# Kernel optimization log

Hardware: AMD Instinct MI355X
Metric: run time of the kernel (lower is better)

Reference implementation:

```python
import jax, jax.numpy as jnp
import numpy as np

B, S1, S2, E, P = 8, 2048, 2048, 1024, 1024


def setup_inputs() -> dict:
    key = jax.random.key(0)
    k1, k2, k3, k4, k5 = jax.random.split(key, 5)
    query = jax.random.normal(k1, (B, S1, E), dtype=jnp.float32)
    key_t = jax.random.normal(k2, (B, S2, E), dtype=jnp.float32)
    value = jax.random.normal(k3, (B, S2, E), dtype=jnp.float32)
    # nn.Linear(E, P): weight (P, E), bias (P), shared by q/k/v per the source
    bound = 1.0 / np.sqrt(E)
    W = jax.random.uniform(k4, (P, E), minval=-bound, maxval=bound, dtype=jnp.float32)
    b = jax.random.uniform(k5, (P,), minval=-bound, maxval=bound, dtype=jnp.float32)
    return {"query": query, "key": key_t, "value": value, "W": W, "b": b}


def reference(query, key, value, W, b):
    # Source applies queries_projection to all three inputs.
    q = jnp.einsum("bse,pe->bsp", query, W) + b  # (B,S1,P)
    k = jnp.einsum("bse,pe->bsp", key, W) + b    # (B,S2,P)
    v = jnp.einsum("bse,pe->bsp", value, W) + b  # (B,S2,P)
    scale = 1.0 / jnp.sqrt(jnp.float32(k.shape[-1]))
    scores = jnp.einsum("bqp,bkp->bqk", q, k) * scale  # (B,S1,S2)
    weights = jax.nn.softmax(scores, axis=-1)
    return jnp.einsum("bqk,bkp->bqp", weights, v)  # (B,S1,P)
```

## Files before the change

kernel.cpp:

```cpp
#include <hip/hip_runtime.h>


typedef unsigned short u16;
typedef __bf16 bf16x8 __attribute__((ext_vector_type(8)));
typedef float f32x4 __attribute__((ext_vector_type(4)));

__device__ __forceinline__ float b2f(u16 u) {
    union { unsigned i; float f; } x; x.i = ((unsigned)u) << 16; return x.f;
}
__device__ __forceinline__ u16 f2b(float f) {
    union { float f; unsigned i; } x; x.f = f;
    unsigned r = x.i + 0x7FFFu + ((x.i >> 16) & 1u);
    return (u16)(r >> 16);
}

__global__ __launch_bounds__(256)
void convert_f32_bf16(const float* __restrict__ src, u16* __restrict__ dst, long n)
{
    long i = ((long)blockIdx.x * 256 + threadIdx.x) * 8;
    if (i >= n) return;
    const float4* s = (const float4*)(src + i);
    float4 a = s[0], b = s[1];
    ushort4 lo, hi;
    lo.x = f2b(a.x); lo.y = f2b(a.y); lo.z = f2b(a.z); lo.w = f2b(a.w);
    hi.x = f2b(b.x); hi.y = f2b(b.y); hi.z = f2b(b.z); hi.w = f2b(b.w);
    *(ushort4*)(dst + i) = lo;
    *(ushort4*)(dst + i + 4) = hi;
}

#define BM 128
#define BN 128
#define BK 64

__global__ __launch_bounds__(256)
void gemm_nt(const void* __restrict__ A0, const void* __restrict__ A1,
             const void* __restrict__ A2in, const u16* __restrict__ Bb,
             void* __restrict__ C, const u16* __restrict__ bias,
             int K, float alpha, int mode, int ldc,
             long zA, long zB, long zC, int pw, int ph)
{
    __shared__ __align__(16) u16 lds[2 * BM * BK];
    u16* As = lds;
    u16* Bs = lds + BM * BK;

    const int z = blockIdx.z;
    const u16* Bp = Bb + zB * z;
    const long coff = zC * z;

    const int aF32 = (mode == 5);
    const u16*  Ab  = aF32 ? nullptr : ((const u16*)A0 + zA * z);
    const float* A32 = aF32 ? (const float*)(z == 0 ? A0 : (z == 1 ? A1 : A2in))
                            : nullptr;
    const int em = aF32 ? (z == 2 ? 2 : 0) : mode;

    int tx = blockIdx.x, ty = blockIdx.y;
    if (pw > 0) {
        const int gx = gridDim.x;
        const int lin = ty * gx + tx;
        const int xcd = lin & 7, i = lin >> 3;
        const int pcols = gx / pw;
        const int pr = xcd / pcols, pc = xcd - pr * pcols;
        tx = pc * pw + (i % pw);
        ty = pr * ph + (i / pw);
    }
    const int bm0 = ty * BM;
    const int bn0 = tx * BN;

    const int tid  = threadIdx.x;
    const int wave = tid >> 6, lane = tid & 63;
    const int wm = wave >> 1, wn = wave & 1;
    const int quad = lane >> 4, l15 = lane & 15;
    const int sw = l15 & 7;

    f32x4 acc[4][4];
#pragma unroll
    for (int i = 0; i < 4; i++)
#pragma unroll
        for (int j = 0; j < 4; j++) acc[i][j] = f32x4{0.f, 0.f, 0.f, 0.f};

    const int stg_r  = wave * 8 + (lane >> 3);
    const int stg_cg = ((lane & 7) ^ (lane >> 3)) * 8;
    const int stg_cl = (lane & 7) * 8;

    for (int kt = 0; kt < K; kt += BK) {
#pragma unroll
        for (int i = 0; i < 4; i++) {
            const int r = i * 32 + stg_r;
            __builtin_amdgcn_global_load_lds(
                (const __attribute__((address_space(1))) void*)(Bp + (long)(bn0 + r) * K + kt + stg_cg),
                (__attribute__((address_space(3))) void*)(Bs + r * BK + stg_cl),
                16, 0, 0);
        }
        if (!aF32) {
#pragma unroll
            for (int i = 0; i < 4; i++) {
                const int r = i * 32 + stg_r;
                __builtin_amdgcn_global_load_lds(
                    (const __attribute__((address_space(1))) void*)(Ab + (long)(bm0 + r) * K + kt + stg_cg),
                    (__attribute__((address_space(3))) void*)(As + r * BK + stg_cl),
                    16, 0, 0);
            }
        } else {
#pragma unroll
            for (int i = 0; i < 4; i++) {
                const int r = i * 32 + stg_r;
                const float* s = A32 + (long)(bm0 + r) * K + kt + stg_cg;
                float4 f0 = *(const float4*)s;
                float4 f1 = *(const float4*)(s + 4);
                uint4 pk;
                pk.x = (unsigned)f2b(f0.x) | ((unsigned)f2b(f0.y) << 16);
                pk.y = (unsigned)f2b(f0.z) | ((unsigned)f2b(f0.w) << 16);
                pk.z = (unsigned)f2b(f1.x) | ((unsigned)f2b(f1.y) << 16);
                pk.w = (unsigned)f2b(f1.z) | ((unsigned)f2b(f1.w) << 16);
                *(uint4*)(As + r * BK + stg_cl) = pk;
            }
        }
        __syncthreads();

#pragma unroll
        for (int kk = 0; kk < 2; kk++) {
            bf16x8 af[4], bb[4];
#pragma unroll
            for (int t = 0; t < 4; t++)
                af[t] = *(const bf16x8*)(As + (wm * 64 + t * 16 + l15) * BK
                                             + (((kk * 4 + quad) ^ sw) * 8));
#pragma unroll
            for (int t = 0; t < 4; t++)
                bb[t] = *(const bf16x8*)(Bs + (wn * 64 + t * 16 + l15) * BK
                                             + (((kk * 4 + quad) ^ sw) * 8));
#pragma unroll
            for (int mt = 0; mt < 4; mt++)
#pragma unroll
                for (int nt = 0; nt < 4; nt++)
                    acc[mt][nt] = __builtin_amdgcn_mfma_f32_16x16x32_bf16(
                        af[mt], bb[nt], acc[mt][nt], 0, 0, 0);
        }
        __syncthreads();
    }

#pragma unroll
    for (int mt = 0; mt < 4; mt++) {
        const int row = bm0 + wm * 64 + mt * 16 + quad * 4;
#pragma unroll
        for (int nt = 0; nt < 4; nt++) {
            const int col = bn0 + wn * 64 + nt * 16 + l15;
            const float bv = bias ? b2f(bias[col]) : 0.f;
            f32x4 v = acc[mt][nt];
            float o0 = alpha * v[0] + bv;
            float o1 = alpha * v[1] + bv;
            float o2 = alpha * v[2] + bv;
            float o3 = alpha * v[3] + bv;
            if (em == 2) {
                ushort4 pk;
                pk.x = f2b(o0); pk.y = f2b(o1); pk.z = f2b(o2); pk.w = f2b(o3);
                *(ushort4*)((u16*)C + coff + ((long)(row >> 11) << 21) + ((long)col << 11) + (row & 2047)) = pk;
            } else if (em == 1) {
                float* Cf = (float*)C + coff;
                Cf[(long)(row + 0) * ldc + col] = o0;
                Cf[(long)(row + 1) * ldc + col] = o1;
                Cf[(long)(row + 2) * ldc + col] = o2;
                Cf[(long)(row + 3) * ldc + col] = o3;
            } else {
                u16* Cb = (u16*)C + coff;
                Cb[(long)(row + 0) * ldc + col] = f2b(o0);
                Cb[(long)(row + 1) * ldc + col] = f2b(o1);
                Cb[(long)(row + 2) * ldc + col] = f2b(o2);
                Cb[(long)(row + 3) * ldc + col] = f2b(o3);
            }
        }
    }
}

__global__ __launch_bounds__(256)
void softmax_rows(u16* __restrict__ S)
{
    const long row = blockIdx.x;
    u16* p = S + (row << 11);
    const int tid = threadIdx.x, wave = tid >> 6, lane = tid & 63;

    union { uint4 q; u16 u[8]; } d;
    d.q = ((const uint4*)p)[tid];
    float v[8];
#pragma unroll
    for (int i = 0; i < 8; i++) v[i] = b2f(d.u[i]);

    float m = v[0];
#pragma unroll
    for (int i = 1; i < 8; i++) m = fmaxf(m, v[i]);
#pragma unroll
    for (int o = 32; o; o >>= 1) m = fmaxf(m, __shfl_xor(m, o, 64));
    __shared__ float redm[4], reds[4];
    if (lane == 0) redm[wave] = m;
    __syncthreads();
    m = fmaxf(fmaxf(redm[0], redm[1]), fmaxf(redm[2], redm[3]));

    float e[8], s = 0.f;
#pragma unroll
    for (int i = 0; i < 8; i++) { e[i] = __expf(v[i] - m); s += e[i]; }
#pragma unroll
    for (int o = 32; o; o >>= 1) s += __shfl_xor(s, o, 64);
    if (lane == 0) reds[wave] = s;
    __syncthreads();
    s = reds[0] + reds[1] + reds[2] + reds[3];

    const float inv = 1.f / s;
#pragma unroll
    for (int i = 0; i < 8; i++) d.u[i] = f2b(e[i] * inv);
    ((uint4*)p)[tid] = d.q;
}

extern "C" void kernel_launch(void* const* d_in, const int* in_sizes, int n_in,
                              void* d_out, int out_size, void* d_ws, size_t ws_size,
                              hipStream_t stream) {
    const float* query = (const float*)d_in[0];
    const float* key   = (const float*)d_in[1];
    const float* value = (const float*)d_in[2];
    const float* W     = (const float*)d_in[3];
    const float* bias  = (const float*)d_in[4];
    float* out = (float*)d_out;

    u16* sc  = (u16*)d_ws;
    u16* Wc  = (u16*)d_ws + 16777216L;
    u16* bc  = Wc + 1048576L;
    u16* qb  = (u16*)d_ws + 33554432L;
    u16* kb  = qb + 16777216L;
    u16* vT  = kb + 16777216L;

    const dim3 blk(256);

    convert_f32_bf16<<<dim3(512), blk, 0, stream>>>(W, Wc, 1048576L);
    convert_f32_bf16<<<dim3(1), blk, 0, stream>>>(bias, bc, 1024L);

    gemm_nt<<<dim3(8, 128, 3), blk, 0, stream>>>(query, key, value, Wc, qb, bc,
        1024, 1.f, 5, 1024, 0, 0, 16777216L, 8, 16);

    gemm_nt<<<dim3(16, 16, 8), blk, 0, stream>>>(qb, nullptr, nullptr, kb, sc, nullptr,
        1024, 0.03125f, 0, 2048, 2048L * 1024, 2048L * 1024, 2048L * 2048, 8, 4);

    softmax_rows<<<dim3(16384), blk, 0, stream>>>(sc);

    gemm_nt<<<dim3(8, 16, 8), blk, 0, stream>>>(sc, nullptr, nullptr, vT, out, nullptr,
        2048, 1.f, 1, 1024, 2048L * 2048, 1024L * 2048, 2048L * 1024, 4, 4);
}
```

Measured before the change: 538.9 us.

## Replace GEMM with 256x256 8-wave pipelined kernel and pre-convert inputs to bf16

Replaces the 128x128 single-buffered GEMM with a 256x256-tile, 512-thread kernel. It double-buffers LDS, interleaves global-to-LDS staging with MFMA quarters under explicit barriers and waitcnts, and raises wave priority around the MFMA blocks. The fused fp32-to-bf16 conversion of the projection A operand is dropped. Instead, query, key and value are each converted to bf16 in a separate pass and then projected by their own launch. This aims at higher MFMA utilisation and better data reuse, at the cost of extra conversion traffic, more launches, and far fewer blocks per GEMM.

After: 490.6 us. -9.0%, faster.

```diff
diff --git a/kernel.cpp b/kernel.cpp
--- a/kernel.cpp
+++ b/kernel.cpp
@@ -28,132 +28,165 @@
     *(ushort4*)(dst + i + 4) = hi;
 }
 
-#define BM 128
-#define BN 128
-#define BK 64
-
-__global__ __launch_bounds__(256)
-void gemm_nt(const void* __restrict__ A0, const void* __restrict__ A1,
-             const void* __restrict__ A2in, const u16* __restrict__ Bb,
-             void* __restrict__ C, const u16* __restrict__ bias,
-             int K, float alpha, int mode, int ldc,
-             long zA, long zB, long zC, int pw, int ph)
+
+#define BARX()   __builtin_amdgcn_s_barrier()
+#define WAITL0() asm volatile("s_waitcnt lgkmcnt(0)" ::: "memory")
+#define WV4()    asm volatile("s_waitcnt vmcnt(4)" ::: "memory")
+#define WV0()    asm volatile("s_waitcnt vmcnt(0)" ::: "memory")
+#define PRIO1()  __builtin_amdgcn_s_setprio(1)
+#define PRIO0()  __builtin_amdgcn_s_setprio(0)
+
+__global__ __launch_bounds__(512, 2)
+void gemm8(const u16* __restrict__ A, const u16* __restrict__ B,
+           void* __restrict__ C, const u16* __restrict__ bias,
+           int K, float alpha, int em, int ldc,
+           long zA, long zB, long zC, int pw, int ph)
 {
-    __shared__ __align__(16) u16 lds[2 * BM * BK];
-    u16* As = lds;
-    u16* Bs = lds + BM * BK;
+    __shared__ __align__(16) u16 lds[65536];
 
     const int z = blockIdx.z;
-    const u16* Bp = Bb + zB * z;
+    const u16* Ap = A + zA * z;
+    const u16* Bp = B + zB * z;
     const long coff = zC * z;
-
-    const int aF32 = (mode == 5);
-    const u16*  Ab  = aF32 ? nullptr : ((const u16*)A0 + zA * z);
-    const float* A32 = aF32 ? (const float*)(z == 0 ? A0 : (z == 1 ? A1 : A2in))
-                            : nullptr;
-    const int em = aF32 ? (z == 2 ? 2 : 0) : mode;
 
     int tx = blockIdx.x, ty = blockIdx.y;
     if (pw > 0) {
         const int gx = gridDim.x;
         const int lin = ty * gx + tx;
-        const int xcd = lin & 7, i = lin >> 3;
+        const int xcd = lin & 7, ii = lin >> 3;
         const int pcols = gx / pw;
         const int pr = xcd / pcols, pc = xcd - pr * pcols;
-        tx = pc * pw + (i % pw);
-        ty = pr * ph + (i / pw);
-    }
-    const int bm0 = ty * BM;
-    const int bn0 = tx * BN;
-
-    const int tid  = threadIdx.x;
+        tx = pc * pw + (ii % pw);
+        ty = pr * ph + (ii / pw);
+    }
+    const int bm0 = ty << 8, bn0 = tx << 8;
+
+    const int tid = threadIdx.x;
     const int wave = tid >> 6, lane = tid & 63;
-    const int wm = wave >> 1, wn = wave & 1;
+    const int wm = wave >> 2, wn = wave & 3;
     const int quad = lane >> 4, l15 = lane & 15;
     const int sw = l15 & 7;
 
-    f32x4 acc[4][4];
-#pragma unroll
-    for (int i = 0; i < 4; i++)
-#pragma unroll
-        for (int j = 0; j < 4; j++) acc[i][j] = f32x4{0.f, 0.f, 0.f, 0.f};
-
-    const int stg_r  = wave * 8 + (lane >> 3);
-    const int stg_cg = ((lane & 7) ^ (lane >> 3)) * 8;
-    const int stg_cl = (lane & 7) * 8;
-
-    for (int kt = 0; kt < K; kt += BK) {
-#pragma unroll
-        for (int i = 0; i < 4; i++) {
-            const int r = i * 32 + stg_r;
-            __builtin_amdgcn_global_load_lds(
-                (const __attribute__((address_space(1))) void*)(Bp + (long)(bn0 + r) * K + kt + stg_cg),
-                (__attribute__((address_space(3))) void*)(Bs + r * BK + stg_cl),
-                16, 0, 0);
-        }
-        if (!aF32) {
-#pragma unroll
-            for (int i = 0; i < 4; i++) {
-                const int r = i * 32 + stg_r;
-                __builtin_amdgcn_global_load_lds(
-                    (const __attribute__((address_space(1))) void*)(Ab + (long)(bm0 + r) * K + kt + stg_cg),
-                    (__attribute__((address_space(3))) void*)(As + r * BK + stg_cl),
-                    16, 0, 0);
-            }
-        } else {
-#pragma unroll
-            for (int i = 0; i < 4; i++) {
-                const int r = i * 32 + stg_r;
-                const float* s = A32 + (long)(bm0 + r) * K + kt + stg_cg;
-                float4 f0 = *(const float4*)s;
-                float4 f1 = *(const float4*)(s + 4);
-                uint4 pk;
-                pk.x = (unsigned)f2b(f0.x) | ((unsigned)f2b(f0.y) << 16);
-                pk.y = (unsigned)f2b(f0.z) | ((unsigned)f2b(f0.w) << 16);
-                pk.z = (unsigned)f2b(f1.x) | ((unsigned)f2b(f1.y) << 16);
-                pk.w = (unsigned)f2b(f1.z) | ((unsigned)f2b(f1.w) << 16);
-                *(uint4*)(As + r * BK + stg_cl) = pk;
-            }
-        }
-        __syncthreads();
-
-#pragma unroll
-        for (int kk = 0; kk < 2; kk++) {
-            bf16x8 af[4], bb[4];
-#pragma unroll
-            for (int t = 0; t < 4; t++)
-                af[t] = *(const bf16x8*)(As + (wm * 64 + t * 16 + l15) * BK
-                                             + (((kk * 4 + quad) ^ sw) * 8));
-#pragma unroll
-            for (int t = 0; t < 4; t++)
-                bb[t] = *(const bf16x8*)(Bs + (wn * 64 + t * 16 + l15) * BK
-                                             + (((kk * 4 + quad) ^ sw) * 8));
-#pragma unroll
-            for (int mt = 0; mt < 4; mt++)
-#pragma unroll
-                for (int nt = 0; nt < 4; nt++)
-                    acc[mt][nt] = __builtin_amdgcn_mfma_f32_16x16x32_bf16(
-                        af[mt], bb[nt], acc[mt][nt], 0, 0, 0);
-        }
-        __syncthreads();
-    }
-
-#pragma unroll
-    for (int mt = 0; mt < 4; mt++) {
-        const int row = bm0 + wm * 64 + mt * 16 + quad * 4;
-#pragma unroll
-        for (int nt = 0; nt < 4; nt++) {
-            const int col = bn0 + wn * 64 + nt * 16 + l15;
+    const int srow = (wave << 3) + (lane >> 3);
+    const int sgc  = (((lane & 7) ^ (lane >> 3)) << 3);
+    const int sdst = (wave << 9) + (lane << 3);
+
+#define STG_A(b, h, kt) do {                                                          \
+    _Pragma("unroll")                                                                 \
+    for (int q_ = 0; q_ < 2; ++q_)                                                    \
+        __builtin_amdgcn_global_load_lds(                                             \
+            (const __attribute__((address_space(1))) void*)(                          \
+                Ap + (long)(bm0 + (h)*128 + q_*64 + srow) * K + (kt) + sgc),          \
+            (__attribute__((address_space(3))) void*)(                                \
+                lds + (b)*32768 + ((h)*128 + q_*64)*64 + sdst),                       \
+            16, 0, 0);                                                                \
+} while (0)
+
+#define STG_B(b, h, kt) do {                                                          \
+    _Pragma("unroll")                                                                 \
+    for (int q_ = 0; q_ < 2; ++q_)                                                    \
+        __builtin_amdgcn_global_load_lds(                                             \
+            (const __attribute__((address_space(1))) void*)(                          \
+                Bp + (long)(bn0 + (h)*128 + q_*64 + srow) * K + (kt) + sgc),          \
+            (__attribute__((address_space(3))) void*)(                                \
+                lds + (b)*32768 + 16384 + ((h)*128 + q_*64)*64 + sdst),               \
+            16, 0, 0);                                                                \
+} while (0)
+
+#define LDA(b, m, kk) (*(const bf16x8*)(lds + (b)*32768 +                             \
+    ((wm << 7) + ((m) << 4) + l15) * 64 + (((((kk) << 2) + quad) ^ sw) << 3)))
+#define LDB(b, n, kk) (*(const bf16x8*)(lds + (b)*32768 + 16384 +                     \
+    ((wn << 6) + ((n) << 4) + l15) * 64 + (((((kk) << 2) + quad) ^ sw) << 3)))
+
+#define RD_A(b, mh) do {                                                              \
+    _Pragma("unroll") for (int mr = 0; mr < 4; ++mr)                                  \
+    _Pragma("unroll") for (int kk = 0; kk < 2; ++kk)                                  \
+        af[mr][kk] = LDA(b, (mh)*4 + mr, kk);                                         \
+} while (0)
+#define RD_B(b, nh) do {                                                              \
+    _Pragma("unroll") for (int j = 0; j < 2; ++j)                                     \
+    _Pragma("unroll") for (int kk = 0; kk < 2; ++kk)                                  \
+        bq[nh][j][kk] = LDB(b, (nh)*2 + j, kk);                                       \
+} while (0)
+
+#define MMAQ(mh, nh) do {                                                             \
+    _Pragma("unroll") for (int mr = 0; mr < 4; ++mr)                                  \
+    _Pragma("unroll") for (int j = 0; j < 2; ++j)                                     \
+    _Pragma("unroll") for (int kk = 0; kk < 2; ++kk)                                  \
+        acc[(mh)*4 + mr][(nh)*2 + j] = __builtin_amdgcn_mfma_f32_16x16x32_bf16(       \
+            af[mr][kk], bq[nh][j][kk], acc[(mh)*4 + mr][(nh)*2 + j], 0, 0, 0);        \
+} while (0)
+
+    f32x4 acc[8][4];
+#pragma unroll
+    for (int m = 0; m < 8; ++m)
+#pragma unroll
+        for (int n = 0; n < 4; ++n) acc[m][n] = f32x4{0.f, 0.f, 0.f, 0.f};
+
+    bf16x8 af[4][2];
+    bf16x8 bq[2][2][2];
+
+    STG_B(0, 0, 0); STG_B(0, 1, 0);
+    STG_A(0, 0, 0); STG_A(0, 1, 0);
+    STG_B(1, 0, 64); STG_B(1, 1, 64);
+    WV4(); BARX();
+
+    const int NI = K >> 7;
+    for (int i = 0; i < NI - 1; ++i) {
+        const int kt0 = i << 7;
+        const int kt1 = kt0 + 64, kt2 = kt0 + 128, kt3 = kt0 + 192;
+        RD_A(0, 0); RD_B(0, 0); STG_A(1, 0, kt1);
+        BARX(); WAITL0(); PRIO1(); MMAQ(0, 0); PRIO0(); BARX();
+        RD_B(0, 1); STG_A(1, 1, kt1);
+        BARX(); WAITL0(); PRIO1(); MMAQ(0, 1); PRIO0(); BARX();
+        RD_A(0, 1); STG_B(0, 0, kt2);
+        BARX(); WAITL0(); PRIO1(); MMAQ(1, 0); PRIO0(); BARX();
+        STG_B(0, 1, kt2);
+        BARX(); PRIO1(); MMAQ(1, 1); PRIO0(); WV4(); BARX();
+        RD_A(1, 0); RD_B(1, 0); STG_A(0, 0, kt2);
+        BARX(); WAITL0(); PRIO1(); MMAQ(0, 0); PRIO0(); BARX();
+        RD_B(1, 1); STG_A(0, 1, kt2);
+        BARX(); WAITL0(); PRIO1(); MMAQ(0, 1); PRIO0(); BARX();
+        RD_A(1, 1); STG_B(1, 0, kt3);
+        BARX(); WAITL0(); PRIO1(); MMAQ(1, 0); PRIO0(); BARX();
+        STG_B(1, 1, kt3);
+        BARX(); PRIO1(); MMAQ(1, 1); PRIO0(); WV4(); BARX();
+    }
+    {
+        const int kt1 = ((NI - 1) << 7) + 64;
+        RD_A(0, 0); RD_B(0, 0); STG_A(1, 0, kt1);
+        BARX(); WAITL0(); PRIO1(); MMAQ(0, 0); PRIO0(); BARX();
+        RD_B(0, 1); STG_A(1, 1, kt1);
+        BARX(); WAITL0(); PRIO1(); MMAQ(0, 1); PRIO0(); BARX();
+        RD_A(0, 1);
+        BARX(); WAITL0(); PRIO1(); MMAQ(1, 0); PRIO0(); BARX();
+        PRIO1(); MMAQ(1, 1); PRIO0(); WV0(); BARX();
+        RD_A(1, 0); RD_B(1, 0);
+        BARX(); WAITL0(); PRIO1(); MMAQ(0, 0); PRIO0(); BARX();
+        RD_B(1, 1);
+        BARX(); WAITL0(); PRIO1(); MMAQ(0, 1); PRIO0(); BARX();
+        RD_A(1, 1);
+        BARX(); WAITL0(); PRIO1(); MMAQ(1, 0); PRIO0(); BARX();
+        PRIO1(); MMAQ(1, 1); PRIO0();
+    }
+
+#pragma unroll
+    for (int m = 0; m < 8; ++m) {
+        const int row = bm0 + (wm << 7) + (m << 4) + (quad << 2);
+#pragma unroll
+        for (int n = 0; n < 4; ++n) {
+            const int col = bn0 + (wn << 6) + (n << 4) + l15;
             const float bv = bias ? b2f(bias[col]) : 0.f;
-            f32x4 v = acc[mt][nt];
-            float o0 = alpha * v[0] + bv;
-            float o1 = alpha * v[1] + bv;
-            float o2 = alpha * v[2] + bv;
-            float o3 = alpha * v[3] + bv;
+            f32x4 v = acc[m][n];
+            const float o0 = alpha * v[0] + bv;
+            const float o1 = alpha * v[1] + bv;
+            const float o2 = alpha * v[2] + bv;
+            const float o3 = alpha * v[3] + bv;
             if (em == 2) {
                 ushort4 pk;
                 pk.x = f2b(o0); pk.y = f2b(o1); pk.z = f2b(o2); pk.w = f2b(o3);
-                *(ushort4*)((u16*)C + coff + ((long)(row >> 11) << 21) + ((long)col << 11) + (row & 2047)) = pk;
+                *(ushort4*)((u16*)C + coff + ((long)(row >> 11) << 21)
+                            + ((long)col << 11) + (row & 2047)) = pk;
             } else if (em == 1) {
                 float* Cf = (float*)C + coff;
                 Cf[(long)(row + 0) * ldc + col] = o0;
@@ -220,25 +253,33 @@
     float* out = (float*)d_out;
 
     u16* sc  = (u16*)d_ws;
+    u16* xc  = (u16*)d_ws;
     u16* Wc  = (u16*)d_ws + 16777216L;
     u16* bc  = Wc + 1048576L;
     u16* qb  = (u16*)d_ws + 33554432L;
     u16* kb  = qb + 16777216L;
     u16* vT  = kb + 16777216L;
 
-    const dim3 blk(256);
-
-    convert_f32_bf16<<<dim3(512), blk, 0, stream>>>(W, Wc, 1048576L);
-    convert_f32_bf16<<<dim3(1), blk, 0, stream>>>(bias, bc, 1024L);
-
-    gemm_nt<<<dim3(8, 128, 3), blk, 0, stream>>>(query, key, value, Wc, qb, bc,
-        1024, 1.f, 5, 1024, 0, 0, 16777216L, 8, 16);
-
-    gemm_nt<<<dim3(16, 16, 8), blk, 0, stream>>>(qb, nullptr, nullptr, kb, sc, nullptr,
-        1024, 0.03125f, 0, 2048, 2048L * 1024, 2048L * 1024, 2048L * 2048, 8, 4);
-
-    softmax_rows<<<dim3(16384), blk, 0, stream>>>(sc);
-
-    gemm_nt<<<dim3(8, 16, 8), blk, 0, stream>>>(sc, nullptr, nullptr, vT, out, nullptr,
-        2048, 1.f, 1, 1024, 2048L * 2048, 1024L * 2048, 2048L * 1024, 4, 4);
-}
+    const dim3 blk2(256), blk5(512);
+
+    convert_f32_bf16<<<dim3(512), blk2, 0, stream>>>(W, Wc, 1048576L);
+    convert_f32_bf16<<<dim3(1),   blk2, 0, stream>>>(bias, bc, 1024L);
+
+    convert_f32_bf16<<<dim3(8192), blk2, 0, stream>>>(query, xc, 16777216L);
+    gemm8<<<dim3(4, 64, 1), blk5, 0, stream>>>(xc, Wc, qb, bc,
+        1024, 1.f, 0, 1024, 0, 0, 0, 4, 8);
+    convert_f32_bf16<<<dim3(8192), blk2, 0, stream>>>(key, xc, 16777216L);
+    gemm8<<<dim3(4, 64, 1), blk5, 0, stream>>>(xc, Wc, kb, bc,
+        1024, 1.f, 0, 1024, 0, 0, 0, 4, 8);
+    convert_f32_bf16<<<dim3(8192), blk2, 0, stream>>>(value, xc, 16777216L);
+    gemm8<<<dim3(4, 64, 1), blk5, 0, stream>>>(xc, Wc, vT, bc,
+        1024, 1.f, 2, 0, 0, 0, 0, 4, 8);
+
+    gemm8<<<dim3(8, 8, 8), blk5, 0, stream>>>(qb, kb, sc, nullptr,
+        1024, 0.03125f, 0, 2048, 2048L * 1024, 2048L * 1024, 2048L * 2048, 8, 1);
+
+    softmax_rows<<<dim3(16384), blk2, 0, stream>>>(sc);
+
+    gemm8<<<dim3(4, 8, 8), blk5, 0, stream>>>(sc, vT, out, nullptr,
+        2048, 1.f, 1, 1024, 2048L * 2048, 1024L * 2048, 2048L * 1024, 4, 1);
+}
```
